# Kernel optimization log

Hardware: AMD Instinct MI355X
Metric: run time of the kernel (lower is better)

The kernel has to match this reference:

```python
import jax, jax.numpy as jnp
import numpy as np
import math

EMBED_DIM = 1024
NUM_HEADS = 16
HEAD_DIM = EMBED_DIM // NUM_HEADS
WINDOW_SIZE = 512
BATCH = 2
SEQ_LEN = 2048


def setup_inputs() -> dict:
    key = jax.random.key(0)
    ks = jax.random.split(key, 9)
    s = 1.0 / math.sqrt(EMBED_DIM)
    inp = {
        "x": jax.random.normal(ks[0], (BATCH, SEQ_LEN, EMBED_DIM), dtype=jnp.float32),
        "Wq": jax.random.normal(ks[1], (EMBED_DIM, EMBED_DIM), dtype=jnp.float32) * s,
        "bq": jnp.zeros((EMBED_DIM,), dtype=jnp.float32),
        "Wk": jax.random.normal(ks[2], (EMBED_DIM, EMBED_DIM), dtype=jnp.float32) * s,
        "bk": jnp.zeros((EMBED_DIM,), dtype=jnp.float32),
        "Wv": jax.random.normal(ks[3], (EMBED_DIM, EMBED_DIM), dtype=jnp.float32) * s,
        "bv": jnp.zeros((EMBED_DIM,), dtype=jnp.float32),
        "Wo": jax.random.normal(ks[4], (EMBED_DIM, EMBED_DIM), dtype=jnp.float32) * s,
        "bo": jnp.zeros((EMBED_DIM,), dtype=jnp.float32),
    }
    return inp


def _sliding_window_mask(seq_len: int, window_size: int) -> jnp.ndarray:
    # mask[i, j] = 0 if |i - j| <= window_size // 2 else -inf
    i = jnp.arange(seq_len)[:, None]
    j = jnp.arange(seq_len)[None, :]
    allowed = jnp.abs(i - j) <= (window_size // 2)
    return jnp.where(allowed, 0.0, -jnp.inf).astype(jnp.float32)


def _split_heads(t):
    b, s, d = t.shape
    return t.reshape(b, s, NUM_HEADS, HEAD_DIM).transpose(0, 2, 1, 3)  # [b,h,s,hd]


def reference(x, Wq, bq, Wk, bk, Wv, bv, Wo, bo):
    b, s, d = x.shape
    q = _split_heads(x @ Wq + bq)
    k = _split_heads(x @ Wk + bk)
    v = _split_heads(x @ Wv + bv)
    # dense QK^T + additive sliding-window mask + softmax + PV (as in source)
    scores = jnp.einsum("bhqd,bhkd->bhqk", q, k) / math.sqrt(HEAD_DIM)
    scores = scores + _sliding_window_mask(s, WINDOW_SIZE)
    probs = jax.nn.softmax(scores, axis=-1)
    attn = jnp.einsum("bhqk,bhkd->bhqd", probs, v)
    attn = attn.transpose(0, 2, 1, 3).reshape(b, s, d)  # merge heads
    return attn @ Wo + bo
```

## Files before the change

### kernel.cpp

```cpp
#include <hip/hip_runtime.h>
#include <math.h>
#include <stdint.h>

#define BATCH 2
#define SEQ   2048
#define EMB   1024
#define NHEADS 16
#define HDIM  64
#define WHALF 256

typedef __attribute__((ext_vector_type(8))) short short8;
typedef __attribute__((ext_vector_type(8))) _Float16 half8;
typedef __attribute__((ext_vector_type(4))) _Float16 half4;
typedef __attribute__((ext_vector_type(4))) float f32x4;

__global__ __launch_bounds__(256)
void cast16_kernel(const float* __restrict__ in, unsigned short* __restrict__ o16, int n)
{
    const int i = (blockIdx.x * 256 + threadIdx.x) * 8;
    if (i >= n) return;
    float4 v0 = *(const float4*)&in[i];
    float4 v1 = *(const float4*)&in[i + 4];
    half8 h;
    h[0] = (_Float16)v0.x; h[1] = (_Float16)v0.y;
    h[2] = (_Float16)v0.z; h[3] = (_Float16)v0.w;
    h[4] = (_Float16)v1.x; h[5] = (_Float16)v1.y;
    h[6] = (_Float16)v1.z; h[7] = (_Float16)v1.w;
    *(half8*)&o16[i] = h;
}

__global__ __launch_bounds__(256)
void wsplit16_t_kernel(const float* __restrict__ W0, const float* __restrict__ W1,
                       const float* __restrict__ W2, const float* __restrict__ W3,
                       unsigned short* __restrict__ o16)
{
    __shared__ float t[32][33];
    const float* W = (blockIdx.z == 0) ? W0 : (blockIdx.z == 1) ? W1
                   : (blockIdx.z == 2) ? W2 : W3;
    const float scale = (blockIdx.z == 0) ? 0.125f : 1.0f;
    const int n0 = blockIdx.x * 32;
    const int k0 = blockIdx.y * 32;
    const int tx = threadIdx.x & 31, ty = threadIdx.x >> 5;
#pragma unroll
    for (int i = 0; i < 4; ++i)
        t[ty + i * 8][tx] = W[(size_t)(k0 + ty + i * 8) * EMB + n0 + tx];
    __syncthreads();
#pragma unroll
    for (int i = 0; i < 4; ++i) {
        float v = t[tx][ty + i * 8] * scale;
        size_t o = (size_t)(blockIdx.z * EMB + n0 + ty + i * 8) * EMB + k0 + tx;
        *(_Float16*)&o16[o] = (_Float16)v;
    }
}

__global__ __launch_bounds__(256)
void bias_cat_kernel(const float* __restrict__ bq, const float* __restrict__ bk,
                     const float* __restrict__ bv, float* __restrict__ out)
{
    const int i = blockIdx.x * 256 + threadIdx.x;
    if (i < 1024)      out[i] = bq[i] * 0.125f;
    else if (i < 2048) out[i] = bk[i - 1024];
    else if (i < 3072) out[i] = bv[i - 2048];
}

#define GLDS(gp, lp) __builtin_amdgcn_global_load_lds(                       \
    (const __attribute__((address_space(1))) void*)(gp),                     \
    (__attribute__((address_space(3))) void*)(lp), 16, 0, 0)

template<int MODE>
__global__ __launch_bounds__(256)
void gemm_f16_kernel(const unsigned short* __restrict__ A,
                     const unsigned short* __restrict__ B,
                     const float* __restrict__ bias,
                     void* __restrict__ C0, void* __restrict__ C1,
                     int ldc, int K)
{
    __shared__ unsigned short sA[128 * 32], sB[128 * 32];

    const int tid = threadIdx.x;
    const int l = tid & 63;
    const int w = tid >> 6;
    const int wm = w >> 1, wn = w & 1;
    const int row0 = blockIdx.y * 128;
    const int col0 = blockIdx.x * 128;

    f32x4 acc[4][4] = {};

    const int sr = tid >> 2;
    const int sk = (tid & 3) * 8;
    const unsigned short* pA = A + (size_t)(row0 + sr) * K + sk;
    const unsigned short* pB = B + (size_t)(col0 + sr) * K + sk;
    const size_t rstep = (size_t)64 * K;

    const int kq = (l >> 4) * 8;
    const int lr = l & 15;

    for (int k0 = 0; k0 < K; k0 += 32) {
        GLDS(pA + k0,         &sA[tid * 8]);
        GLDS(pA + rstep + k0, &sA[2048 + tid * 8]);
        GLDS(pB + k0,         &sB[tid * 8]);
        GLDS(pB + rstep + k0, &sB[2048 + tid * 8]);
        __syncthreads();

        half8 af[4], bf[4];
#pragma unroll
        for (int f = 0; f < 4; ++f) {
            af[f] = *(const half8*)&sA[(wm * 64 + f * 16 + lr) * 32 + kq];
            bf[f] = *(const half8*)&sB[(wn * 64 + f * 16 + lr) * 32 + kq];
        }
#pragma unroll
        for (int mf = 0; mf < 4; ++mf)
#pragma unroll
            for (int nf = 0; nf < 4; ++nf)
                acc[mf][nf] = __builtin_amdgcn_mfma_f32_16x16x32_f16(af[mf], bf[nf], acc[mf][nf], 0, 0, 0);
        __syncthreads();
    }

    const int lq = l >> 4;
#pragma unroll
    for (int nf = 0; nf < 4; ++nf) {
        const int c = wn * 64 + nf * 16 + lr;
        const float bv = bias[col0 + c];
#pragma unroll
        for (int mf = 0; mf < 4; ++mf) {
            const int r = row0 + wm * 64 + mf * 16 + lq * 4;
            if (MODE == 0) {
#pragma unroll
                for (int i = 0; i < 4; ++i)
                    ((float*)C0)[(size_t)(r + i) * ldc + col0 + c] = acc[mf][nf][i] + bv;
            } else if (col0 < 2048) {
#pragma unroll
                for (int i = 0; i < 4; ++i)
                    ((_Float16*)C0)[(size_t)(r + i) * 2048 + col0 + c] =
                        (_Float16)(acc[mf][nf][i] + bv);
            } else {
                half4 pk;
#pragma unroll
                for (int i = 0; i < 4; ++i) pk[i] = (_Float16)(acc[mf][nf][i] + bv);
                const int vb = r >> 11, s = r & 2047;
                *(half4*)((_Float16*)C1 + ((size_t)(vb * 1024 + (col0 - 2048 + c))) * 2048 + s) = pk;
            }
        }
    }
}

#define AP 66

__global__ __launch_bounds__(256)
void attn_f16_kernel(const unsigned short* __restrict__ QKb,
                     const unsigned short* __restrict__ Vt,
                     unsigned short* __restrict__ Oa)
{
    __shared__ unsigned short Qs[64 * AP], Ks[64 * AP], Vs[64 * AP], Ps[64 * AP];

    const int tid = threadIdx.x;
    const int gid = blockIdx.x;
    const int X = gid & 7, rest = gid >> 3;
    const int hg = rest & 3, tile = rest >> 2;
    const int bh = X * 4 + hg;
    const int b = bh >> 4, h = bh & 15;
    const int q0 = tile * 64;

    const int l = tid & 63, w = tid >> 6;
    const int lr = l & 15, g = l >> 4;

    const size_t rowbase = (size_t)b * SEQ;

    {
        const int r = tid >> 2, sg = (tid & 3) * 16;
        const unsigned short* src = QKb + (rowbase + q0 + r) * 2048 + h * HDIM + sg;
        *(short8*)&Qs[r * AP + sg]     = *(const short8*)src;
        *(short8*)&Qs[r * AP + sg + 8] = *(const short8*)(src + 8);
    }
    __syncthreads();

    half8 qa0 = *(const half8*)&Qs[(w * 16 + lr) * AP + g * 8];
    half8 qa1 = *(const half8*)&Qs[(w * 16 + lr) * AP + 32 + g * 8];

    f32x4 o[4] = {};
    float m_[4], l_[4];
#pragma unroll
    for (int i = 0; i < 4; ++i) { m_[i] = -1e30f; l_[i] = 0.0f; }

    const int c_begin = (q0 >= WHALF) ? 0 : (WHALF - q0) >> 6;
    int c_end = (SEQ + 192 - q0) >> 6; if (c_end > 8) c_end = 8;

    for (int c = c_begin; c <= c_end; ++c) {
        const int cs = q0 - WHALF + c * 64;

        {
            const int r = tid >> 2, sg = (tid & 3) * 16;
            const unsigned short* ks = QKb + (rowbase + cs + r) * 2048 + 1024 + h * HDIM + sg;
            *(short8*)&Ks[r * AP + sg]     = *(const short8*)ks;
            *(short8*)&Ks[r * AP + sg + 8] = *(const short8*)(ks + 8);
            const unsigned short* vs = Vt + ((size_t)(b * 1024 + h * HDIM + r)) * 2048 + cs + sg;
            *(short8*)&Vs[r * AP + sg]     = *(const short8*)vs;
            *(short8*)&Vs[r * AP + sg + 8] = *(const short8*)(vs + 8);
        }
        __syncthreads();

        f32x4 sc[4] = {};
#pragma unroll
        for (int kf = 0; kf < 4; ++kf) {
            half8 b0 = *(const half8*)&Ks[(kf * 16 + lr) * AP + g * 8];
            half8 b1 = *(const half8*)&Ks[(kf * 16 + lr) * AP + 32 + g * 8];
            sc[kf] = __builtin_amdgcn_mfma_f32_16x16x32_f16(qa0, b0, sc[kf], 0, 0, 0);
            sc[kf] = __builtin_amdgcn_mfma_f32_16x16x32_f16(qa1, b1, sc[kf], 0, 0, 0);
        }

        if (c == 0) {
#pragma unroll
            for (int kf = 0; kf < 4; ++kf) {
                const int j = cs + kf * 16 + lr;
#pragma unroll
                for (int i = 0; i < 4; ++i) {
                    const int q = q0 + w * 16 + g * 4 + i;
                    if (j < q - WHALF) sc[kf][i] = -1e30f;
                }
            }
        } else if (c == 8) {
#pragma unroll
            for (int kf = 0; kf < 4; ++kf) {
                const int j = cs + kf * 16 + lr;
#pragma unroll
                for (int i = 0; i < 4; ++i) {
                    const int q = q0 + w * 16 + g * 4 + i;
                    if (j > q + WHALF) sc[kf][i] = -1e30f;
                }
            }
        }

        float cm[4], alpha[4], rs[4];
#pragma unroll
        for (int i = 0; i < 4; ++i) {
            float v = fmaxf(fmaxf(sc[0][i], sc[1][i]), fmaxf(sc[2][i], sc[3][i]));
            v = fmaxf(v, __shfl_xor(v, 1));
            v = fmaxf(v, __shfl_xor(v, 2));
            v = fmaxf(v, __shfl_xor(v, 4));
            v = fmaxf(v, __shfl_xor(v, 8));
            cm[i] = v;
        }
#pragma unroll
        for (int i = 0; i < 4; ++i) {
            const float mn = fmaxf(fmaxf(m_[i], cm[i]), -1e4f);
            alpha[i] = __expf(m_[i] - mn);
            m_[i] = mn;
            rs[i] = 0.0f;
        }
#pragma unroll
        for (int kf = 0; kf < 4; ++kf)
#pragma unroll
            for (int i = 0; i < 4; ++i) {
                const float p = __expf(sc[kf][i] - m_[i]);
                rs[i] += p;
                *(_Float16*)&Ps[(w * 16 + g * 4 + i) * AP + kf * 16 + lr] = (_Float16)p;
            }
#pragma unroll
        for (int i = 0; i < 4; ++i) {
            float v = rs[i];
            v += __shfl_xor(v, 1);
            v += __shfl_xor(v, 2);
            v += __shfl_xor(v, 4);
            v += __shfl_xor(v, 8);
            l_[i] = l_[i] * alpha[i] + v;
        }
#pragma unroll
        for (int df = 0; df < 4; ++df)
#pragma unroll
            for (int i = 0; i < 4; ++i) o[df][i] *= alpha[i];

        half8 pa0 = *(const half8*)&Ps[(w * 16 + lr) * AP + g * 8];
        half8 pa1 = *(const half8*)&Ps[(w * 16 + lr) * AP + 32 + g * 8];
#pragma unroll
        for (int df = 0; df < 4; ++df) {
            half8 vb0 = *(const half8*)&Vs[(df * 16 + lr) * AP + g * 8];
            half8 vb1 = *(const half8*)&Vs[(df * 16 + lr) * AP + 32 + g * 8];
            o[df] = __builtin_amdgcn_mfma_f32_16x16x32_f16(pa0, vb0, o[df], 0, 0, 0);
            o[df] = __builtin_amdgcn_mfma_f32_16x16x32_f16(pa1, vb1, o[df], 0, 0, 0);
        }
        __syncthreads();
    }

    float inv[4];
#pragma unroll
    for (int i = 0; i < 4; ++i) inv[i] = 1.0f / l_[i];
#pragma unroll
    for (int df = 0; df < 4; ++df)
#pragma unroll
        for (int i = 0; i < 4; ++i) {
            const float v = o[df][i] * inv[i];
            const size_t off = (rowbase + q0 + w * 16 + g * 4 + i) * 1024
                             + h * HDIM + df * 16 + lr;
            *(_Float16*)&Oa[off] = (_Float16)v;
        }
}

#define BM 64
#define BN 64
#define BK 16

__global__ __launch_bounds__(256)
void gemm_bias_kernel(const float* __restrict__ A, const float* __restrict__ W,
                      const float* __restrict__ bias, float* __restrict__ C,
                      int M, int N, int K)
{
    __shared__ float As[BK][BM + 4];
    __shared__ float Bs[BK][BN + 4];
    const int tid = threadIdx.x;
    const int tx = tid & 15, ty = tid >> 4;
    const int row0 = blockIdx.y * BM;
    const int col0 = blockIdx.x * BN;
    float acc[4][4] = {};
    const int ar = tid >> 2;
    const int ak = (tid & 3) * 4;
    const int br = tid >> 4;
    const int bc = (tid & 15) * 4;
    for (int k0 = 0; k0 < K; k0 += BK) {
        float4 a = *(const float4*)&A[(size_t)(row0 + ar) * K + k0 + ak];
        float4 b = *(const float4*)&W[(size_t)(k0 + br) * N + col0 + bc];
        As[ak + 0][ar] = a.x; As[ak + 1][ar] = a.y;
        As[ak + 2][ar] = a.z; As[ak + 3][ar] = a.w;
        *(float4*)&Bs[br][bc] = b;
        __syncthreads();
#pragma unroll
        for (int kk = 0; kk < BK; ++kk) {
            float4 av = *(const float4*)&As[kk][ty * 4];
            float4 bv = *(const float4*)&Bs[kk][tx * 4];
            float aa[4] = {av.x, av.y, av.z, av.w};
            float bb[4] = {bv.x, bv.y, bv.z, bv.w};
#pragma unroll
            for (int i = 0; i < 4; ++i)
#pragma unroll
                for (int j = 0; j < 4; ++j)
                    acc[i][j] = fmaf(aa[i], bb[j], acc[i][j]);
        }
        __syncthreads();
    }
    const float4 bvec = *(const float4*)&bias[col0 + tx * 4];
    const float bb[4] = {bvec.x, bvec.y, bvec.z, bvec.w};
#pragma unroll
    for (int i = 0; i < 4; ++i) {
        float4 oo;
        oo.x = acc[i][0] + bb[0]; oo.y = acc[i][1] + bb[1];
        oo.z = acc[i][2] + bb[2]; oo.w = acc[i][3] + bb[3];
        *(float4*)&C[(size_t)(row0 + ty * 4 + i) * N + col0 + tx * 4] = oo;
    }
}

#define QT 32
#define KT 64

__global__ __launch_bounds__(256)
void attn_kernel(const float* __restrict__ Qm, int ldq,
                 const float* __restrict__ Km, int ldk,
                 const float* __restrict__ Vm, int ldv,
                 float* __restrict__ Om, int ldo)
{
    __shared__ float Qs[QT][HDIM + 4];
    __shared__ float KVs[KT][HDIM + 4];
    __shared__ float Ps[QT][KT + 1];
    __shared__ float red[8][QT];
    __shared__ float m_s[QT], l_s[QT], alpha_s[QT];
    const int tid = threadIdx.x;
    const int b  = blockIdx.y / NHEADS;
    const int h  = blockIdx.y % NHEADS;
    const int q0 = blockIdx.x * QT;
    const int r  = tid & 31;
    const int cg = tid >> 5;
    const int d0 = cg * 8;
    {
        const int qr = tid >> 3;
        const int qd = (tid & 7) * 8;
        const float* src = Qm + (size_t)(b * SEQ + q0 + qr) * ldq + h * HDIM + qd;
        *(float4*)&Qs[qr][qd]     = *(const float4*)(src);
        *(float4*)&Qs[qr][qd + 4] = *(const float4*)(src + 4);
    }
    if (tid < QT) { m_s[tid] = -1e30f; l_s[tid] = 0.0f; }
    __syncthreads();
    float qreg[HDIM];
#pragma unroll
    for (int d4 = 0; d4 < HDIM; d4 += 4) {
        float4 t = *(const float4*)&Qs[r][d4];
        qreg[d4] = t.x; qreg[d4 + 1] = t.y; qreg[d4 + 2] = t.z; qreg[d4 + 3] = t.w;
    }
    float o[8] = {};
    const int iq = q0 + r;
    int lo = q0 - WHALF; if (lo < 0) lo = 0;
    const int cs0 = lo & ~(KT - 1);
    int hi = q0 + QT + WHALF; if (hi > SEQ) hi = SEQ;
    const int nch = (hi - cs0 + KT - 1) / KT;
    const int kr0 = tid >> 4;
    const int kc  = (tid & 15) * 4;
    for (int ch = 0; ch < nch; ++ch) {
        const int cs = cs0 + ch * KT;
#pragma unroll
        for (int r4 = 0; r4 < 4; ++r4) {
            const int row = kr0 + r4 * 16;
            const int j = cs + row;
            float4 v = make_float4(0.f, 0.f, 0.f, 0.f);
            if (j < SEQ)
                v = *(const float4*)&Km[(size_t)(b * SEQ + j) * ldk + h * HDIM + kc];
            *(float4*)&KVs[row][kc] = v;
        }
        __syncthreads();
        float s[8];
#pragma unroll
        for (int cc = 0; cc < 8; ++cc) {
            const int cidx = d0 + cc;
            float acc = 0.0f;
#pragma unroll
            for (int d4 = 0; d4 < HDIM; d4 += 4) {
                float4 kv = *(const float4*)&KVs[cidx][d4];
                acc = fmaf(qreg[d4],     kv.x, acc);
                acc = fmaf(qreg[d4 + 1], kv.y, acc);
                acc = fmaf(qreg[d4 + 2], kv.z, acc);
                acc = fmaf(qreg[d4 + 3], kv.w, acc);
            }
            const int j = cs + cidx;
            const bool valid = (j < SEQ) && (j >= iq - WHALF) && (j <= iq + WHALF);
            s[cc] = valid ? acc * 0.125f : -1e30f;
        }
        float lm = s[0];
#pragma unroll
        for (int cc = 1; cc < 8; ++cc) lm = fmaxf(lm, s[cc]);
        red[cg][r] = lm;
        __syncthreads();
        if (tid < QT) {
            float m = m_s[tid];
            float mc = red[0][tid];
#pragma unroll
            for (int g2 = 1; g2 < 8; ++g2) mc = fmaxf(mc, red[g2][tid]);
            const float mn = fmaxf(m, mc);
            alpha_s[tid] = __expf(m - mn);
            m_s[tid] = mn;
        }
        __syncthreads();
        const float mn = m_s[r];
        float ls = 0.0f;
#pragma unroll
        for (int cc = 0; cc < 8; ++cc) {
            const float p = __expf(s[cc] - mn);
            Ps[r][d0 + cc] = p;
            ls += p;
        }
        red[cg][r] = ls;
        __syncthreads();
        if (tid < QT) {
            float sum = red[0][tid];
#pragma unroll
            for (int g2 = 1; g2 < 8; ++g2) sum += red[g2][tid];
            l_s[tid] = l_s[tid] * alpha_s[tid] + sum;
        }
#pragma unroll
        for (int r4 = 0; r4 < 4; ++r4) {
            const int row = kr0 + r4 * 16;
            const int j = cs + row;
            float4 v = make_float4(0.f, 0.f, 0.f, 0.f);
            if (j < SEQ)
                v = *(const float4*)&Vm[(size_t)(b * SEQ + j) * ldv + h * HDIM + kc];
            *(float4*)&KVs[row][kc] = v;
        }
        {
            const float al = alpha_s[r];
#pragma unroll
            for (int dd = 0; dd < 8; ++dd) o[dd] *= al;
        }
        __syncthreads();
        for (int j = 0; j < KT; ++j) {
            const float p = Ps[r][j];
            float4 v0 = *(const float4*)&KVs[j][d0];
            float4 v1 = *(const float4*)&KVs[j][d0 + 4];
            o[0] = fmaf(p, v0.x, o[0]); o[1] = fmaf(p, v0.y, o[1]);
            o[2] = fmaf(p, v0.z, o[2]); o[3] = fmaf(p, v0.w, o[3]);
            o[4] = fmaf(p, v1.x, o[4]); o[5] = fmaf(p, v1.y, o[5]);
            o[6] = fmaf(p, v1.z, o[6]); o[7] = fmaf(p, v1.w, o[7]);
        }
        __syncthreads();
    }
    const float inv = 1.0f / l_s[r];
    float4 o0, o1;
    o0.x = o[0] * inv; o0.y = o[1] * inv; o0.z = o[2] * inv; o0.w = o[3] * inv;
    o1.x = o[4] * inv; o1.y = o[5] * inv; o1.z = o[6] * inv; o1.w = o[7] * inv;
    float* dst = Om + (size_t)(b * SEQ + q0 + r) * ldo + h * HDIM + d0;
    *(float4*)dst       = o0;
    *(float4*)(dst + 4) = o1;
}

extern "C" void kernel_launch(void* const* d_in, const int* in_sizes, int n_in,
                              void* d_out, int out_size, void* d_ws, size_t ws_size,
                              hipStream_t stream)
{
    const float* x  = (const float*)d_in[0];
    const float* Wq = (const float*)d_in[1];
    const float* bq = (const float*)d_in[2];
    const float* Wk = (const float*)d_in[3];
    const float* bk = (const float*)d_in[4];
    const float* Wv = (const float*)d_in[5];
    const float* bv = (const float*)d_in[6];
    const float* Wo = (const float*)d_in[7];
    const float* bo = (const float*)d_in[8];
    float* out = (float*)d_out;

    const int M = BATCH * SEQ;
    const size_t MK = (size_t)M * EMB;

    const size_t need = ((size_t)40 << 20) + 16384;
    dim3 blk(256);

    if (ws_size >= need) {
        unsigned short* Wh  = (unsigned short*)d_ws;
        unsigned short* xh  = Wh + (size_t)4096 * EMB;
        unsigned short* QKb = xh + MK;
        unsigned short* Vt  = QKb + (size_t)4096 * 2048;
        unsigned short* Oa  = xh;
        float* bias_cat = (float*)((char*)d_ws + ((size_t)40 << 20));

        hipLaunchKernelGGL(cast16_kernel, dim3((int)(MK / (256 * 8))), blk, 0, stream,
                           x, xh, (int)MK);
        hipLaunchKernelGGL(wsplit16_t_kernel, dim3(32, 32, 4), blk, 0, stream,
                           Wq, Wk, Wv, Wo, Wh);
        hipLaunchKernelGGL(bias_cat_kernel, dim3(12), blk, 0, stream, bq, bk, bv, bias_cat);

        hipLaunchKernelGGL((gemm_f16_kernel<1>), dim3(24, 32), blk, 0, stream,
                           xh, Wh, bias_cat, (void*)QKb, (void*)Vt, 0, EMB);

        hipLaunchKernelGGL(attn_f16_kernel, dim3(1024), blk, 0, stream, QKb, Vt, Oa);

        hipLaunchKernelGGL((gemm_f16_kernel<0>), dim3(8, 32), blk, 0, stream,
                           Oa, Wh + (size_t)3072 * EMB, bo, (void*)out, nullptr, EMB, EMB);
    } else {
        float* Qb = (float*)d_ws;
        float* Kb = Qb + MK;
        float* Vb = out;
        dim3 ggrid(EMB / BN, M / BM);
        hipLaunchKernelGGL(gemm_bias_kernel, ggrid, blk, 0, stream, x, Wq, bq, Qb, M, EMB, EMB);
        hipLaunchKernelGGL(gemm_bias_kernel, ggrid, blk, 0, stream, x, Wk, bk, Kb, M, EMB, EMB);
        hipLaunchKernelGGL(gemm_bias_kernel, ggrid, blk, 0, stream, x, Wv, bv, Vb, M, EMB, EMB);
        hipLaunchKernelGGL(attn_kernel, dim3(SEQ / QT, BATCH * NHEADS), blk, 0, stream,
                           Qb, EMB, Kb, EMB, Vb, EMB, Qb, EMB);
        hipLaunchKernelGGL(gemm_bias_kernel, ggrid, blk, 0, stream, Qb, Wo, bo, out, M, EMB, EMB);
    }
}
```

Measured before the change: 208.6 us.

## Stage GEMM epilogues through LDS, use 64-row output GEMM, transpose attention scores

The QKV projection epilogue now writes results into a padded LDS tile and then emits coalesced 16-byte stores, for both the row-major Q/K output and the transposed V output, instead of scattered 2-byte and 8-byte stores. The output projection uses a new 64-row tile kernel, which doubles the number of blocks to fill more compute units. The attention kernel swaps the operands of the QK^T MFMA so each lane holds one query row. This turns the row max and sum reductions into two cross-lane shuffles and lets P be written to LDS as packed half4 values. The cost is a large extra LDS buffer (about 34 KB) in the QKV GEMM, which may lower occupancy, plus extra shuffles to redistribute alpha and l across lanes.

```diff
diff --git a/kernel.cpp b/kernel.cpp
--- a/kernel.cpp
+++ b/kernel.cpp
@@ -67,15 +67,17 @@
     (const __attribute__((address_space(1))) void*)(gp),                     \
     (__attribute__((address_space(3))) void*)(lp), 16, 0, 0)
 
-template<int MODE>
-__global__ __launch_bounds__(256)
-void gemm_f16_kernel(const unsigned short* __restrict__ A,
-                     const unsigned short* __restrict__ B,
-                     const float* __restrict__ bias,
-                     void* __restrict__ C0, void* __restrict__ C1,
-                     int ldc, int K)
+#define TRS 136
+
+__global__ __launch_bounds__(256)
+void gemm_f16_qkv_kernel(const unsigned short* __restrict__ A,
+                         const unsigned short* __restrict__ B,
+                         const float* __restrict__ bias,
+                         _Float16* __restrict__ QK,
+                         _Float16* __restrict__ Vt, int K)
 {
     __shared__ unsigned short sA[128 * 32], sB[128 * 32];
+    __shared__ _Float16 tr[128 * TRS];
 
     const int tid = threadIdx.x;
     const int l = tid & 63;
@@ -94,6 +96,7 @@
 
     const int kq = (l >> 4) * 8;
     const int lr = l & 15;
+    const int lq = l >> 4;
 
     for (int k0 = 0; k0 < K; k0 += 32) {
         GLDS(pA + k0,         &sA[tid * 8]);
@@ -116,30 +119,107 @@
         __syncthreads();
     }
 
+    if (col0 < 2048) {
+#pragma unroll
+        for (int nf = 0; nf < 4; ++nf) {
+            const int c = wn * 64 + nf * 16 + lr;
+            const float bv = bias[col0 + c];
+#pragma unroll
+            for (int mf = 0; mf < 4; ++mf) {
+                const int rl = wm * 64 + mf * 16 + lq * 4;
+#pragma unroll
+                for (int i = 0; i < 4; ++i)
+                    tr[(rl + i) * TRS + c] = (_Float16)(acc[mf][nf][i] + bv);
+            }
+        }
+        __syncthreads();
+        const int r = tid >> 1, seg = (tid & 1) * 64;
+        _Float16* dst = QK + (size_t)(row0 + r) * 2048 + col0 + seg;
+#pragma unroll
+        for (int t = 0; t < 8; ++t)
+            *(half8*)&dst[t * 8] = *(const half8*)&tr[r * TRS + seg + t * 8];
+    } else {
+#pragma unroll
+        for (int nf = 0; nf < 4; ++nf) {
+            const int c = wn * 64 + nf * 16 + lr;
+            const float bv = bias[col0 + c];
+#pragma unroll
+            for (int mf = 0; mf < 4; ++mf) {
+                const int rl = wm * 64 + mf * 16 + lq * 4;
+#pragma unroll
+                for (int i = 0; i < 4; ++i)
+                    tr[c * TRS + rl + i] = (_Float16)(acc[mf][nf][i] + bv);
+            }
+        }
+        __syncthreads();
+        const int c = tid >> 1, seg = (tid & 1) * 64;
+        const int vb = row0 >> 11;
+        const int s0 = (row0 & 2047) + seg;
+        _Float16* dst = Vt + ((size_t)(vb * 1024 + (col0 - 2048) + c)) * 2048 + s0;
+#pragma unroll
+        for (int t = 0; t < 8; ++t)
+            *(half8*)&dst[t * 8] = *(const half8*)&tr[c * TRS + seg + t * 8];
+    }
+}
+
+__global__ __launch_bounds__(256)
+void gemm_f16_m64_kernel(const unsigned short* __restrict__ A,
+                         const unsigned short* __restrict__ B,
+                         const float* __restrict__ bias,
+                         float* __restrict__ C, int ldc, int K)
+{
+    __shared__ unsigned short sA[64 * 32], sB[128 * 32];
+
+    const int tid = threadIdx.x;
+    const int l = tid & 63;
+    const int w = tid >> 6;
+    const int wm = w >> 1, wn = w & 1;
+    const int row0 = blockIdx.y * 64;
+    const int col0 = blockIdx.x * 128;
+
+    f32x4 acc[2][4] = {};
+
+    const int sr = tid >> 2;
+    const int sk = (tid & 3) * 8;
+    const unsigned short* pA = A + (size_t)(row0 + sr) * K + sk;
+    const unsigned short* pB = B + (size_t)(col0 + sr) * K + sk;
+    const size_t rstep = (size_t)64 * K;
+
+    const int kq = (l >> 4) * 8;
+    const int lr = l & 15;
     const int lq = l >> 4;
+
+    for (int k0 = 0; k0 < K; k0 += 32) {
+        GLDS(pA + k0,         &sA[tid * 8]);
+        GLDS(pB + k0,         &sB[tid * 8]);
+        GLDS(pB + rstep + k0, &sB[2048 + tid * 8]);
+        __syncthreads();
+
+        half8 af[2], bf[4];
+#pragma unroll
+        for (int f = 0; f < 2; ++f)
+            af[f] = *(const half8*)&sA[(wm * 32 + f * 16 + lr) * 32 + kq];
+#pragma unroll
+        for (int f = 0; f < 4; ++f)
+            bf[f] = *(const half8*)&sB[(wn * 64 + f * 16 + lr) * 32 + kq];
+#pragma unroll
+        for (int mf = 0; mf < 2; ++mf)
+#pragma unroll
+            for (int nf = 0; nf < 4; ++nf)
+                acc[mf][nf] = __builtin_amdgcn_mfma_f32_16x16x32_f16(af[mf], bf[nf], acc[mf][nf], 0, 0, 0);
+        __syncthreads();
+    }
+
 #pragma unroll
     for (int nf = 0; nf < 4; ++nf) {
         const int c = wn * 64 + nf * 16 + lr;
         const float bv = bias[col0 + c];
 #pragma unroll
-        for (int mf = 0; mf < 4; ++mf) {
-            const int r = row0 + wm * 64 + mf * 16 + lq * 4;
-            if (MODE == 0) {
-#pragma unroll
-                for (int i = 0; i < 4; ++i)
-                    ((float*)C0)[(size_t)(r + i) * ldc + col0 + c] = acc[mf][nf][i] + bv;
-            } else if (col0 < 2048) {
-#pragma unroll
-                for (int i = 0; i < 4; ++i)
-                    ((_Float16*)C0)[(size_t)(r + i) * 2048 + col0 + c] =
-                        (_Float16)(acc[mf][nf][i] + bv);
-            } else {
-                half4 pk;
-#pragma unroll
-                for (int i = 0; i < 4; ++i) pk[i] = (_Float16)(acc[mf][nf][i] + bv);
-                const int vb = r >> 11, s = r & 2047;
-                *(half4*)((_Float16*)C1 + ((size_t)(vb * 1024 + (col0 - 2048 + c))) * 2048 + s) = pk;
-            }
+        for (int mf = 0; mf < 2; ++mf) {
+            const int r = row0 + wm * 32 + mf * 16 + lq * 4;
+#pragma unroll
+            for (int i = 0; i < 4; ++i)
+                C[(size_t)(r + i) * ldc + col0 + c] = acc[mf][nf][i] + bv;
         }
     }
 }
@@ -178,9 +258,8 @@
     half8 qa1 = *(const half8*)&Qs[(w * 16 + lr) * AP + 32 + g * 8];
 
     f32x4 o[4] = {};
-    float m_[4], l_[4];
-#pragma unroll
-    for (int i = 0; i < 4; ++i) { m_[i] = -1e30f; l_[i] = 0.0f; }
+    float m_ = -1e30f, l_ = 0.0f;
+    const int q = q0 + w * 16 + lr;
 
     const int c_begin = (q0 >= WHALF) ? 0 : (WHALF - q0) >> 6;
     int c_end = (SEQ + 192 - q0) >> 6; if (c_end > 8) c_end = 8;
@@ -202,72 +281,66 @@
         f32x4 sc[4] = {};
 #pragma unroll
         for (int kf = 0; kf < 4; ++kf) {
-            half8 b0 = *(const half8*)&Ks[(kf * 16 + lr) * AP + g * 8];
-            half8 b1 = *(const half8*)&Ks[(kf * 16 + lr) * AP + 32 + g * 8];
-            sc[kf] = __builtin_amdgcn_mfma_f32_16x16x32_f16(qa0, b0, sc[kf], 0, 0, 0);
-            sc[kf] = __builtin_amdgcn_mfma_f32_16x16x32_f16(qa1, b1, sc[kf], 0, 0, 0);
+            half8 a0 = *(const half8*)&Ks[(kf * 16 + lr) * AP + g * 8];
+            half8 a1 = *(const half8*)&Ks[(kf * 16 + lr) * AP + 32 + g * 8];
+            sc[kf] = __builtin_amdgcn_mfma_f32_16x16x32_f16(a0, qa0, sc[kf], 0, 0, 0);
+            sc[kf] = __builtin_amdgcn_mfma_f32_16x16x32_f16(a1, qa1, sc[kf], 0, 0, 0);
         }
 
         if (c == 0) {
 #pragma unroll
-            for (int kf = 0; kf < 4; ++kf) {
-                const int j = cs + kf * 16 + lr;
+            for (int kf = 0; kf < 4; ++kf)
 #pragma unroll
                 for (int i = 0; i < 4; ++i) {
-                    const int q = q0 + w * 16 + g * 4 + i;
-                    if (j < q - WHALF) sc[kf][i] = -1e30f;
+                    const int key = cs + kf * 16 + g * 4 + i;
+                    if (key < q - WHALF) sc[kf][i] = -1e30f;
                 }
+        } else if (c == 8) {
+#pragma unroll
+            for (int kf = 0; kf < 4; ++kf)
+#pragma unroll
+                for (int i = 0; i < 4; ++i) {
+                    const int key = cs + kf * 16 + g * 4 + i;
+                    if (key > q + WHALF) sc[kf][i] = -1e30f;
+                }
+        }
+
+        float cm = sc[0][0];
+#pragma unroll
+        for (int kf = 0; kf < 4; ++kf)
+#pragma unroll
+            for (int i = 0; i < 4; ++i) cm = fmaxf(cm, sc[kf][i]);
+        cm = fmaxf(cm, __shfl_xor(cm, 16));
+        cm = fmaxf(cm, __shfl_xor(cm, 32));
+
+        const float mn = fmaxf(fmaxf(m_, cm), -1e4f);
+        const float alpha = __expf(m_ - mn);
+        m_ = mn;
+
+        float rs = 0.0f;
+#pragma unroll
+        for (int kf = 0; kf < 4; ++kf) {
+            half4 pk;
+#pragma unroll
+            for (int i = 0; i < 4; ++i) {
+                const float p = __expf(sc[kf][i] - mn);
+                rs += p;
+                pk[i] = (_Float16)p;
             }
-        } else if (c == 8) {
-#pragma unroll
-            for (int kf = 0; kf < 4; ++kf) {
-                const int j = cs + kf * 16 + lr;
-#pragma unroll
-                for (int i = 0; i < 4; ++i) {
-                    const int q = q0 + w * 16 + g * 4 + i;
-                    if (j > q + WHALF) sc[kf][i] = -1e30f;
-                }
-            }
-        }
-
-        float cm[4], alpha[4], rs[4];
-#pragma unroll
-        for (int i = 0; i < 4; ++i) {
-            float v = fmaxf(fmaxf(sc[0][i], sc[1][i]), fmaxf(sc[2][i], sc[3][i]));
-            v = fmaxf(v, __shfl_xor(v, 1));
-            v = fmaxf(v, __shfl_xor(v, 2));
-            v = fmaxf(v, __shfl_xor(v, 4));
-            v = fmaxf(v, __shfl_xor(v, 8));
-            cm[i] = v;
-        }
-#pragma unroll
-        for (int i = 0; i < 4; ++i) {
-            const float mn = fmaxf(fmaxf(m_[i], cm[i]), -1e4f);
-            alpha[i] = __expf(m_[i] - mn);
-            m_[i] = mn;
-            rs[i] = 0.0f;
-        }
-#pragma unroll
-        for (int kf = 0; kf < 4; ++kf)
-#pragma unroll
-            for (int i = 0; i < 4; ++i) {
-                const float p = __expf(sc[kf][i] - m_[i]);
-                rs[i] += p;
-                *(_Float16*)&Ps[(w * 16 + g * 4 + i) * AP + kf * 16 + lr] = (_Float16)p;
-            }
-#pragma unroll
-        for (int i = 0; i < 4; ++i) {
-            float v = rs[i];
-            v += __shfl_xor(v, 1);
-            v += __shfl_xor(v, 2);
-            v += __shfl_xor(v, 4);
-            v += __shfl_xor(v, 8);
-            l_[i] = l_[i] * alpha[i] + v;
-        }
+            *(half4*)&Ps[(w * 16 + lr) * AP + kf * 16 + g * 4] = pk;
+        }
+        rs += __shfl_xor(rs, 16);
+        rs += __shfl_xor(rs, 32);
+        l_ = l_ * alpha + rs;
+
+        float al[4];
+#pragma unroll
+        for (int i = 0; i < 4; ++i)
+            al[i] = __shfl(alpha, (l & 48) | (g * 4 + i));
 #pragma unroll
         for (int df = 0; df < 4; ++df)
 #pragma unroll
-            for (int i = 0; i < 4; ++i) o[df][i] *= alpha[i];
+            for (int i = 0; i < 4; ++i) o[df][i] *= al[i];
 
         half8 pa0 = *(const half8*)&Ps[(w * 16 + lr) * AP + g * 8];
         half8 pa1 = *(const half8*)&Ps[(w * 16 + lr) * AP + 32 + g * 8];
@@ -281,14 +354,15 @@
         __syncthreads();
     }
 
-    float inv[4];
-#pragma unroll
-    for (int i = 0; i < 4; ++i) inv[i] = 1.0f / l_[i];
+    float invl[4];
+#pragma unroll
+    for (int i = 0; i < 4; ++i)
+        invl[i] = 1.0f / __shfl(l_, (l & 48) | (g * 4 + i));
 #pragma unroll
     for (int df = 0; df < 4; ++df)
 #pragma unroll
         for (int i = 0; i < 4; ++i) {
-            const float v = o[df][i] * inv[i];
+            const float v = o[df][i] * invl[i];
             const size_t off = (rowbase + q0 + w * 16 + g * 4 + i) * 1024
                              + h * HDIM + df * 16 + lr;
             *(_Float16*)&Oa[off] = (_Float16)v;
@@ -521,13 +595,13 @@
                            Wq, Wk, Wv, Wo, Wh);
         hipLaunchKernelGGL(bias_cat_kernel, dim3(12), blk, 0, stream, bq, bk, bv, bias_cat);
 
-        hipLaunchKernelGGL((gemm_f16_kernel<1>), dim3(24, 32), blk, 0, stream,
-                           xh, Wh, bias_cat, (void*)QKb, (void*)Vt, 0, EMB);
+        hipLaunchKernelGGL(gemm_f16_qkv_kernel, dim3(24, 32), blk, 0, stream,
+                           xh, Wh, bias_cat, (_Float16*)QKb, (_Float16*)Vt, EMB);
 
         hipLaunchKernelGGL(attn_f16_kernel, dim3(1024), blk, 0, stream, QKb, Vt, Oa);
 
-        hipLaunchKernelGGL((gemm_f16_kernel<0>), dim3(8, 32), blk, 0, stream,
-                           Oa, Wh + (size_t)3072 * EMB, bo, (void*)out, nullptr, EMB, EMB);
+        hipLaunchKernelGGL(gemm_f16_m64_kernel, dim3(8, 64), blk, 0, stream,
+                           Oa, Wh + (size_t)3072 * EMB, bo, out, EMB, EMB);
     } else {
         float* Qb = (float*)d_ws;
         float* Kb = Qb + MK;
```

Result: no change. 208.2 us (-0.2%).
